# Kernel tuning notes

Measured on AMD Instinct MI355X. Metric: run time of the kernel, lower is better.

The kernel has to match this reference:

```python
import jax, jax.numpy as jnp
import numpy as np

B, IN_DIM, NUM_BINS, EMBED_DIM = 32768, 64, 10, 64
EPS = 1e-6


def setup_inputs() -> dict:
    key = jax.random.key(0)
    k_x, k_logit, k_emb, k_w, k_b = jax.random.split(key, 5)
    x = jax.random.normal(k_x, (B, IN_DIM), dtype=jnp.float32)
    bin_logits = jax.random.normal(k_logit, (NUM_BINS,), dtype=jnp.float32)
    embed = jax.random.normal(k_emb, (NUM_BINS, EMBED_DIM), dtype=jnp.float32)
    # nn.Linear default init: U(-1/sqrt(fan_in), 1/sqrt(fan_in))
    bound = 1.0 / np.sqrt(EMBED_DIM)
    W = jax.random.uniform(k_w, (EMBED_DIM, EMBED_DIM), dtype=jnp.float32, minval=-bound, maxval=bound)
    b = jax.random.uniform(k_b, (EMBED_DIM,), dtype=jnp.float32, minval=-bound, maxval=bound)
    return {"x": x, "bin_logits": bin_logits, "embed": embed, "W": W, "b": b}


def reference(x, bin_logits, embed, W, b):
    # per-column min-max normalize over the batch dim
    x_min = x.min(axis=0)
    x_max = x.max(axis=0)
    x_norm = (x - x_min) / (x_max - x_min + EPS)            # [B, IN_DIM]
    # soft bin edges
    bins = jnp.cumsum(jax.nn.softmax(bin_logits))            # [NUM_BINS]
    # torch.bucketize(right=False) == searchsorted side='left'
    idx = jnp.clip(jnp.searchsorted(bins, x_norm, side='left'), 0, NUM_BINS - 1)
    e = embed[idx]                                           # [B, IN_DIM, EMBED_DIM]
    # lin(e).sum(dim=1) == (sum_n e) @ W.T + IN_DIM * b  (linear is affine)
    out = jnp.einsum('bne,fe->bf', e, W) + jnp.float32(IN_DIM) * b
    return out
```

## Files before the change

kernel.cpp:

```cpp
#include <hip/hip_runtime.h>
#include <cmath>

#define B_ROWS    32768
#define IN_DIM    64
#define NUM_BINS  10
#define EMBED_DIM 64
#define NBLK1     256

__device__ __forceinline__ unsigned f2key(float f) {
    unsigned u = __float_as_uint(f);
    return (u & 0x80000000u) ? ~u : (u | 0x80000000u);
}
__device__ __forceinline__ float key2f(unsigned k) {
    unsigned u = (k & 0x80000000u) ? (k ^ 0x80000000u) : ~k;
    return __uint_as_float(u);
}

__global__ __launch_bounds__(256) void minmax_kernel(const float* __restrict__ x,
                                                     unsigned* __restrict__ ws) {
    __shared__ unsigned smin[IN_DIM], smax[IN_DIM];
    int t = threadIdx.x;
    if (t < IN_DIM) { smin[t] = 0xFFFFFFFFu; smax[t] = 0u; }
    __syncthreads();

    const float4* x4 = (const float4*)x;
    const int total = B_ROWS * IN_DIM / 4;
    const int stride = NBLK1 * 256;
    int g = blockIdx.x * 256 + t;
    int cg = (g & 15) * 4;

    float mn0 =  INFINITY, mn1 =  INFINITY, mn2 =  INFINITY, mn3 =  INFINITY;
    float mx0 = -INFINITY, mx1 = -INFINITY, mx2 = -INFINITY, mx3 = -INFINITY;
    #pragma unroll
    for (int i = g; i < total; i += stride) {
        float4 v = x4[i];
        mn0 = fminf(mn0, v.x); mx0 = fmaxf(mx0, v.x);
        mn1 = fminf(mn1, v.y); mx1 = fmaxf(mx1, v.y);
        mn2 = fminf(mn2, v.z); mx2 = fmaxf(mx2, v.z);
        mn3 = fminf(mn3, v.w); mx3 = fmaxf(mx3, v.w);
    }
    atomicMin(&smin[cg + 0], f2key(mn0)); atomicMax(&smax[cg + 0], f2key(mx0));
    atomicMin(&smin[cg + 1], f2key(mn1)); atomicMax(&smax[cg + 1], f2key(mx1));
    atomicMin(&smin[cg + 2], f2key(mn2)); atomicMax(&smax[cg + 2], f2key(mx2));
    atomicMin(&smin[cg + 3], f2key(mn3)); atomicMax(&smax[cg + 3], f2key(mx3));
    __syncthreads();
    if (t < 2 * IN_DIM) {
        unsigned v = (t < IN_DIM) ? smin[t] : smax[t - IN_DIM];
        ws[blockIdx.x * 128 + t] = v;
    }
}

__global__ __launch_bounds__(1024) void main_kernel(
    const float* __restrict__ x, const float* __restrict__ logits,
    const float* __restrict__ embed, const float* __restrict__ W,
    const float* __restrict__ bias, const unsigned* __restrict__ ws,
    float* __restrict__ out)
{
    __shared__ float smn[IN_DIM], sden[IN_DIM], sbias[EMBED_DIM];
    __shared__ float sbins[NUM_BINS];
    __shared__ float sM[NUM_BINS * EMBED_DIM];
    __shared__ unsigned pmin[16][IN_DIM], pmax[16][IN_DIM];

    int t = threadIdx.x;

    {
        int col = t & 63, chunk = t >> 6;
        unsigned kmin = 0xFFFFFFFFu, kmax = 0u;
        #pragma unroll
        for (int b = chunk; b < NBLK1; b += 16) {
            unsigned lo = ws[b * 128 + col];
            unsigned hi = ws[b * 128 + 64 + col];
            kmin = min(kmin, lo);
            kmax = max(kmax, hi);
        }
        pmin[chunk][col] = kmin;
        pmax[chunk][col] = kmax;
    }
    __syncthreads();
    if (t < IN_DIM) {
        unsigned kmin = 0xFFFFFFFFu, kmax = 0u;
        #pragma unroll
        for (int c = 0; c < 16; c++) {
            kmin = min(kmin, pmin[c][t]);
            kmax = max(kmax, pmax[c][t]);
        }
        float mn = key2f(kmin);
        float mx = key2f(kmax);
        smn[t]  = mn;
        sden[t] = mx - mn + 1e-6f;
        sbias[t] = 64.0f * bias[t];
    }
    if (t == 0) {
        float l[NUM_BINS], e[NUM_BINS];
        float m = -INFINITY;
        #pragma unroll
        for (int i = 0; i < NUM_BINS; i++) { l[i] = logits[i]; m = fmaxf(m, l[i]); }
        float s = 0.0f;
        #pragma unroll
        for (int i = 0; i < NUM_BINS; i++) { e[i] = expf(l[i] - m); s += e[i]; }
        float c = 0.0f;
        #pragma unroll
        for (int i = 0; i < NUM_BINS; i++) { c += e[i] / s; sbins[i] = c; }
    }
    for (int id = t; id < NUM_BINS * EMBED_DIM; id += 1024) {
        int k = id >> 6, f = id & 63;
        const float* er = embed + k * EMBED_DIM;
        const float* wr = W + f * EMBED_DIM;
        float acc = 0.0f;
        #pragma unroll 8
        for (int e = 0; e < EMBED_DIM; e++) acc += er[e] * wr[e];
        sM[id] = acc;
    }
    __syncthreads();

    int w = t >> 6;
    int lane = t & 63;
    float cmn = smn[lane], cden = sden[lane], cbias = sbias[lane];

    #pragma unroll
    for (int r = blockIdx.x * 16 + w; r < B_ROWS; r += 256 * 16) {
        float xv = x[r * IN_DIM + lane];
        float xn = (xv - cmn) / cden;
        int idx = 0;
        #pragma unroll
        for (int k = 0; k < NUM_BINS; k++) idx += (sbins[k] < xn) ? 1 : 0;
        if (idx > NUM_BINS - 1) idx = NUM_BINS - 1;

        float acc = cbias;
        #pragma unroll
        for (int k = 0; k < NUM_BINS; k++) {
            unsigned long long msk = __ballot(idx == k);
            acc = fmaf((float)__popcll(msk), sM[k * EMBED_DIM + lane], acc);
        }
        out[r * EMBED_DIM + lane] = acc;
    }
}

extern "C" void kernel_launch(void* const* d_in, const int* in_sizes, int n_in,
                              void* d_out, int out_size, void* d_ws, size_t ws_size,
                              hipStream_t stream) {
    const float* x      = (const float*)d_in[0];
    const float* logits = (const float*)d_in[1];
    const float* embed  = (const float*)d_in[2];
    const float* W      = (const float*)d_in[3];
    const float* bias   = (const float*)d_in[4];
    float* out = (float*)d_out;

    unsigned* ws = (unsigned*)d_ws;

    minmax_kernel<<<NBLK1, 256, 0, stream>>>(x, ws);
    main_kernel<<<256, 1024, 0, stream>>>(x, logits, embed, W, bias, ws, out);
}
```

Baseline: 84.76 us.

## Fuse min-max and main kernels into one cooperative launch with grid sync

```diff
diff --git a/kernel.cpp b/kernel.cpp
--- a/kernel.cpp
+++ b/kernel.cpp
@@ -1,11 +1,14 @@
 #include <hip/hip_runtime.h>
+#include <hip/hip_cooperative_groups.h>
 #include <cmath>
+
+namespace cg = cooperative_groups;
 
 #define B_ROWS    32768
 #define IN_DIM    64
 #define NUM_BINS  10
 #define EMBED_DIM 64
-#define NBLK1     256
+#define NBLK      256
 
 __device__ __forceinline__ unsigned f2key(float f) {
     unsigned u = __float_as_uint(f);
@@ -16,62 +19,53 @@
     return __uint_as_float(u);
 }
 
-__global__ __launch_bounds__(256) void minmax_kernel(const float* __restrict__ x,
-                                                     unsigned* __restrict__ ws) {
-    __shared__ unsigned smin[IN_DIM], smax[IN_DIM];
-    int t = threadIdx.x;
-    if (t < IN_DIM) { smin[t] = 0xFFFFFFFFu; smax[t] = 0u; }
-    __syncthreads();
-
-    const float4* x4 = (const float4*)x;
-    const int total = B_ROWS * IN_DIM / 4;
-    const int stride = NBLK1 * 256;
-    int g = blockIdx.x * 256 + t;
-    int cg = (g & 15) * 4;
-
-    float mn0 =  INFINITY, mn1 =  INFINITY, mn2 =  INFINITY, mn3 =  INFINITY;
-    float mx0 = -INFINITY, mx1 = -INFINITY, mx2 = -INFINITY, mx3 = -INFINITY;
-    #pragma unroll
-    for (int i = g; i < total; i += stride) {
-        float4 v = x4[i];
-        mn0 = fminf(mn0, v.x); mx0 = fmaxf(mx0, v.x);
-        mn1 = fminf(mn1, v.y); mx1 = fmaxf(mx1, v.y);
-        mn2 = fminf(mn2, v.z); mx2 = fmaxf(mx2, v.z);
-        mn3 = fminf(mn3, v.w); mx3 = fmaxf(mx3, v.w);
-    }
-    atomicMin(&smin[cg + 0], f2key(mn0)); atomicMax(&smax[cg + 0], f2key(mx0));
-    atomicMin(&smin[cg + 1], f2key(mn1)); atomicMax(&smax[cg + 1], f2key(mx1));
-    atomicMin(&smin[cg + 2], f2key(mn2)); atomicMax(&smax[cg + 2], f2key(mx2));
-    atomicMin(&smin[cg + 3], f2key(mn3)); atomicMax(&smax[cg + 3], f2key(mx3));
-    __syncthreads();
-    if (t < 2 * IN_DIM) {
-        unsigned v = (t < IN_DIM) ? smin[t] : smax[t - IN_DIM];
-        ws[blockIdx.x * 128 + t] = v;
-    }
-}
-
-__global__ __launch_bounds__(1024) void main_kernel(
+__global__ __launch_bounds__(1024) void fused_kernel(
     const float* __restrict__ x, const float* __restrict__ logits,
     const float* __restrict__ embed, const float* __restrict__ W,
-    const float* __restrict__ bias, const unsigned* __restrict__ ws,
+    const float* __restrict__ bias, unsigned* __restrict__ ws,
     float* __restrict__ out)
 {
-    __shared__ float smn[IN_DIM], sden[IN_DIM], sbias[EMBED_DIM];
+    __shared__ unsigned smin[IN_DIM], smax[IN_DIM];
+    __shared__ float sden[IN_DIM], smn[IN_DIM], sbias[EMBED_DIM];
     __shared__ float sbins[NUM_BINS];
     __shared__ float sM[NUM_BINS * EMBED_DIM];
     __shared__ unsigned pmin[16][IN_DIM], pmax[16][IN_DIM];
 
     int t = threadIdx.x;
+    int b = blockIdx.x;
+
+    if (t < IN_DIM) { smin[t] = 0xFFFFFFFFu; smax[t] = 0u; }
+    __syncthreads();
+
+    const float4* x4 = (const float4*)x;
+    int g = b * 1024 + t;
+    float4 v0 = x4[g];
+    float4 v1 = x4[g + 262144];
+    int cg4 = (g & 15) * 4;
+
+    atomicMin(&smin[cg4 + 0], f2key(fminf(v0.x, v1.x)));
+    atomicMax(&smax[cg4 + 0], f2key(fmaxf(v0.x, v1.x)));
+    atomicMin(&smin[cg4 + 1], f2key(fminf(v0.y, v1.y)));
+    atomicMax(&smax[cg4 + 1], f2key(fmaxf(v0.y, v1.y)));
+    atomicMin(&smin[cg4 + 2], f2key(fminf(v0.z, v1.z)));
+    atomicMax(&smax[cg4 + 2], f2key(fmaxf(v0.z, v1.z)));
+    atomicMin(&smin[cg4 + 3], f2key(fminf(v0.w, v1.w)));
+    atomicMax(&smax[cg4 + 3], f2key(fmaxf(v0.w, v1.w)));
+    __syncthreads();
+    if (t < 2 * IN_DIM) {
+        unsigned v = (t < IN_DIM) ? smin[t] : smax[t - IN_DIM];
+        ws[b * 128 + t] = v;
+    }
+
+    cg::this_grid().sync();
 
     {
         int col = t & 63, chunk = t >> 6;
         unsigned kmin = 0xFFFFFFFFu, kmax = 0u;
         #pragma unroll
-        for (int b = chunk; b < NBLK1; b += 16) {
-            unsigned lo = ws[b * 128 + col];
-            unsigned hi = ws[b * 128 + 64 + col];
-            kmin = min(kmin, lo);
-            kmax = max(kmax, hi);
+        for (int blk = chunk; blk < NBLK; blk += 16) {
+            kmin = min(kmin, ws[blk * 128 + col]);
+            kmax = max(kmax, ws[blk * 128 + 64 + col]);
         }
         pmin[chunk][col] = kmin;
         pmax[chunk][col] = kmax;
@@ -117,22 +111,28 @@
     int lane = t & 63;
     float cmn = smn[lane], cden = sden[lane], cbias = sbias[lane];
 
+    int base = b * 64 + w * 4;
     #pragma unroll
-    for (int r = blockIdx.x * 16 + w; r < B_ROWS; r += 256 * 16) {
-        float xv = x[r * IN_DIM + lane];
-        float xn = (xv - cmn) / cden;
-        int idx = 0;
+    for (int half = 0; half < 2; half++) {
+        int r0 = base + half * 16384;
         #pragma unroll
-        for (int k = 0; k < NUM_BINS; k++) idx += (sbins[k] < xn) ? 1 : 0;
-        if (idx > NUM_BINS - 1) idx = NUM_BINS - 1;
+        for (int q = 0; q < 4; q++) {
+            int r = r0 + q;
+            float xv = x[r * IN_DIM + lane];
+            float xn = (xv - cmn) / cden;
+            int idx = 0;
+            #pragma unroll
+            for (int k = 0; k < NUM_BINS; k++) idx += (sbins[k] < xn) ? 1 : 0;
+            if (idx > NUM_BINS - 1) idx = NUM_BINS - 1;
 
-        float acc = cbias;
-        #pragma unroll
-        for (int k = 0; k < NUM_BINS; k++) {
-            unsigned long long msk = __ballot(idx == k);
-            acc = fmaf((float)__popcll(msk), sM[k * EMBED_DIM + lane], acc);
+            float acc = cbias;
+            #pragma unroll
+            for (int k = 0; k < NUM_BINS; k++) {
+                unsigned long long msk = __ballot(idx == k);
+                acc = fmaf((float)__popcll(msk), sM[k * EMBED_DIM + lane], acc);
+            }
+            out[r * EMBED_DIM + lane] = acc;
         }
-        out[r * EMBED_DIM + lane] = acc;
     }
 }
 
@@ -145,9 +145,10 @@
     const float* W      = (const float*)d_in[3];
     const float* bias   = (const float*)d_in[4];
     float* out = (float*)d_out;
-
     unsigned* ws = (unsigned*)d_ws;
 
-    minmax_kernel<<<NBLK1, 256, 0, stream>>>(x, ws);
-    main_kernel<<<256, 1024, 0, stream>>>(x, logits, embed, W, bias, ws, out);
+    void* args[] = {(void*)&x, (void*)&logits, (void*)&embed, (void*)&W,
+                    (void*)&bias, (void*)&ws, (void*)&out};
+    hipLaunchCooperativeKernel((void*)fused_kernel, dim3(NBLK), dim3(1024),
+                               args, 0, stream);
 }
```

Measured after the change: 115.3 us. +36.0%, slower.
